# Optimization experiments

Measured on AMD Instinct MI355X. Metric: run time of the kernel, lower is better.

Reference implementation:

```python
import jax, jax.numpy as jnp
import numpy as np

BETA = 0.25  # commitment loss weight


def setup_inputs() -> dict:
    key = jax.random.key(0)
    ks = jax.random.split(key, 6)
    B, H, W, C = 16, 64, 64, 128
    x = jax.random.normal(ks[0], (B, H, W, C), dtype=jnp.float32)
    # dictionaries: sizes 2^6 .. 2^9 (from num_embeddings=[64,512]),
    # keras RandomUniform default init in (-0.05, 0.05)
    dicts = {}
    for i, n_emb in enumerate([64, 128, 256, 512]):
        dicts[f"dict{i}"] = jax.random.uniform(
            ks[i + 1], (C, n_emb), dtype=jnp.float32, minval=-0.05, maxval=0.05)
    vq_alpha = jnp.asarray(1.0, dtype=jnp.float32)
    vq_gamma = jnp.full((4,), 0.25, dtype=jnp.float32)  # 1/num_dictionaries
    return {"x": x, **dicts, "vq_alpha": vq_alpha, "vq_gamma": vq_gamma}


def _vq_pass(flat, D):
    # flat: [N, C], D: [C, K]. Squared-euclidean distances then argmin.
    dist = (jnp.sum(flat * flat, axis=1, keepdims=True)
            + jnp.sum(D * D, axis=0)[None, :]
            - 2.0 * (flat @ D))  # [N, K]
    idx = jnp.argmin(dist, axis=1)  # [N]
    # one_hot @ D.T  ==  gather rows of D.T
    return jnp.take(D.T, idx, axis=0)  # [N, C]


def reference(x, dict0, dict1, dict2, dict3, vq_alpha, vq_gamma):
    dicts = [dict0, dict1, dict2, dict3]
    C = x.shape[-1]
    flat = x.reshape(-1, C)  # [N, C]
    weighted_q = jnp.zeros_like(x)
    dictionary_loss = jnp.asarray(0.0, x.dtype)
    commitment_loss = jnp.asarray(0.0, x.dtype)
    for i, D in enumerate(dicts):
        q = (vq_alpha * _vq_pass(flat, D)).reshape(x.shape)
        weighted_q = weighted_q + vq_gamma[i] * q
        dictionary_loss += vq_gamma[i] * jnp.mean(
            jnp.square(jax.lax.stop_gradient(x) - q))
        commitment_loss += vq_gamma[i] * jnp.mean(
            jnp.square(x - jax.lax.stop_gradient(q)))
    loss = dictionary_loss + BETA * commitment_loss
    # straight-through estimator
    out = x + jax.lax.stop_gradient(weighted_q - x)
    return out, loss
```

## Files before the change

### kernel.cpp

```cpp
#include <hip/hip_runtime.h>

#define CDIM 128
#define NC   8388608

typedef __attribute__((ext_vector_type(8)))  short bf8v;
typedef __attribute__((ext_vector_type(16))) float f32x16;


__device__ __forceinline__ void bsplit(float v, short& h, short& lo) {
  unsigned u = __float_as_uint(v);
  unsigned hb = (u + 0x7fffu + ((u >> 16) & 1u)) >> 16;
  float hf = __uint_as_float(hb << 16);
  float lf = v - hf;
  unsigned u2 = __float_as_uint(lf);
  unsigned lb = (u2 + 0x7fffu + ((u2 >> 16) & 1u)) >> 16;
  h = (short)hb; lo = (short)lb;
}

__global__ void vq_prep(const float* __restrict__ D0, const float* __restrict__ D1,
                        const float* __restrict__ D2, const float* __restrict__ D3,
                        float* __restrict__ nrm, float* __restrict__ DT,
                        bf8v* __restrict__ Bph, bf8v* __restrict__ Bpl) {
  const int b = blockIdx.x;
  if (b < 60) {
    int g = b * 256 + threadIdx.x;
    int T = g >> 9, c = (g >> 6) & 7, l = g & 63;
    int col = T * 32 + (l & 31);
    int k0 = c * 16 + (l >> 5) * 8;
    const float* D; int K, cb;
    if (col < 64)       { D = D0; K = 64;  cb = col; }
    else if (col < 192) { D = D1; K = 128; cb = col - 64; }
    else if (col < 448) { D = D2; K = 256; cb = col - 192; }
    else                { D = D3; K = 512; cb = col - 448; }
    short h0,h1,h2,h3,h4,h5,h6,h7, q0,q1,q2,q3,q4,q5,q6,q7;
    bsplit(D[(k0+0)*K + cb], h0, q0);
    bsplit(D[(k0+1)*K + cb], h1, q1);
    bsplit(D[(k0+2)*K + cb], h2, q2);
    bsplit(D[(k0+3)*K + cb], h3, q3);
    bsplit(D[(k0+4)*K + cb], h4, q4);
    bsplit(D[(k0+5)*K + cb], h5, q5);
    bsplit(D[(k0+6)*K + cb], h6, q6);
    bsplit(D[(k0+7)*K + cb], h7, q7);
    Bph[g] = (bf8v){h0,h1,h2,h3,h4,h5,h6,h7};
    Bpl[g] = (bf8v){q0,q1,q2,q3,q4,q5,q6,q7};
  } else {
    int g = (b - 60) * 256 + threadIdx.x;
    if (g >= 960) return;
    const float* D; int K, k; float* T;
    if (g < 64)       { D = D0; K = 64;  k = g;       T = DT; }
    else if (g < 192) { D = D1; K = 128; k = g - 64;  T = DT + 8192; }
    else if (g < 448) { D = D2; K = 256; k = g - 192; T = DT + 24576; }
    else              { D = D3; K = 512; k = g - 448; T = DT + 57344; }
    float s = 0.f;
    for (int c = 0; c < 128; ++c) { float v = D[c*K+k]; s = fmaf(v,v,s); T[k*128+c] = v; }
    nrm[g] = s;
  }
}

#define MK8(U0, U1, HD, LD) { \
  short h0,h1,h2,h3,h4,h5,h6,h7, q0,q1,q2,q3,q4,q5,q6,q7; \
  bsplit(U0.x,h0,q0); bsplit(U0.y,h1,q1); bsplit(U0.z,h2,q2); bsplit(U0.w,h3,q3); \
  bsplit(U1.x,h4,q4); bsplit(U1.y,h5,q5); bsplit(U1.z,h6,q6); bsplit(U1.w,h7,q7); \
  HD = (bf8v){h0,h1,h2,h3,h4,h5,h6,h7}; \
  LD = (bf8v){q0,q1,q2,q3,q4,q5,q6,q7}; }

#define MFMA32(AC, AF, BF) AC = __builtin_amdgcn_mfma_f32_32x32x16_bf16((AF), (BF), (AC), 0, 0, 0)

#define PF_T(TT) { \
  const bf8v* __restrict__ gh = Bph + (TT) * 512; \
  const bf8v* __restrict__ gl = Bpl + (TT) * 512; \
  pf0 = gh[t]; pf1 = gh[256 + t]; pf2 = gl[t]; pf3 = gl[256 + t]; }

#define STORE_T(BF) { \
  BL[BF][t] = pf0; BL[BF][256 + t] = pf1; BL[BF][512 + t] = pf2; BL[BF][768 + t] = pf3; }

#define COMPUTE_T(T, BF) { \
  f32x16 ae = zero16, ao = zero16; \
  _Pragma("unroll") \
  for (int cp = 0; cp < 4; ++cp) { \
    const int ce = 2*cp, co = 2*cp+1; \
    bf8v bhe = BL[BF][ce*64 + l]; bf8v bho = BL[BF][co*64 + l]; \
    bf8v ble = BL[BF][512 + ce*64 + l]; bf8v blo = BL[BF][512 + co*64 + l]; \
    MFMA32(ae, Ah[ce], bhe); MFMA32(ao, Ah[co], bho); \
    MFMA32(ae, Al[ce], bhe); MFMA32(ao, Al[co], bho); \
    MFMA32(ae, Ah[ce], ble); MFMA32(ao, Ah[co], blo); \
  } \
  f32x16 sv = ae + ao; \
  const float nv = nrm_g[(T)*32 + (l & 31)]; \
  const int colT = (T)*32 + (l & 31); \
  _Pragma("unroll") \
  for (int r = 0; r < 16; ++r) { \
    float c0 = fmaf(-2.f, sv[r], nv); \
    if (c0 < bc[r]) { bc[r] = c0; bk[r] = colT; } } }

#define ROUND_T(T) { \
  if ((T) < 29) { \
    STORE_T(((T) + 1) & 1); \
    const int TN = ((T) + 2 <= 29) ? (T) + 2 : 29; \
    PF_T(TN); \
  } \
  COMPUTE_T(T, (T) & 1) \
  __syncthreads(); }

#define FLUSHG(DICTID, BASE, GAM) { \
  _Pragma("unroll") \
  for (int r = 0; r < 16; ++r) { \
    float b0 = bc[r]; int K0 = bk[r]; \
    _Pragma("unroll") \
    for (int m = 1; m <= 16; m <<= 1) { \
      float pb = __shfl_xor(b0, m); int pk = __shfl_xor(K0, m); \
      if (pb < b0 || (pb == b0 && pk < K0)) { b0 = pb; K0 = pk; } } \
    if ((l & 31) == 0) { \
      const int ro = (r & 3) + 8 * (r >> 2) + 4 * hl; \
      keys[((rowbase + ro) << 2) | (DICTID)] = K0 - (BASE); \
      const float nst = nrm_g[K0]; \
       \
      lossacc = fmaf((GAM) * a, fmaf(am1, nst, b0), lossacc); } \
    bc[r] = 1e30f; bk[r] = 0; } }

__global__ __launch_bounds__(256, 2) void vq_mfma(
    const float* __restrict__ x,
    const bf8v* __restrict__ Bph, const bf8v* __restrict__ Bpl,
    const float* __restrict__ nrm_g,
    const float* __restrict__ alpha_p, const float* __restrict__ gamma_p,
    int* __restrict__ keys, float* __restrict__ partials)
{
  __shared__ bf8v  BL[2][1024];
  __shared__ float lossW[4];

  const int t = threadIdx.x;
  const int w = t >> 6, l = t & 63;
  const int hl = l >> 5;
  const int rowbase = blockIdx.x * 128 + w * 32;

  const float a   = alpha_p[0];
  const float am1 = a - 1.f;
  const float g0 = gamma_p[0], g1 = gamma_p[1], g2 = gamma_p[2], g3 = gamma_p[3];
  const float gsum = g0 + g1 + g2 + g3;

  bf8v Ah[8], Al[8];
  float xsqh = 0.f;
  {
    const float* __restrict__ xr = x + (size_t)(rowbase + (l & 31)) * CDIM + hl * 8;
    #pragma unroll
    for (int c = 0; c < 8; ++c) {
      float4 u0 = *(const float4*)(xr + c * 16);
      float4 u1 = *(const float4*)(xr + c * 16 + 4);
      xsqh = fmaf(u0.x,u0.x, xsqh); xsqh = fmaf(u0.y,u0.y, xsqh);
      xsqh = fmaf(u0.z,u0.z, xsqh); xsqh = fmaf(u0.w,u0.w, xsqh);
      xsqh = fmaf(u1.x,u1.x, xsqh); xsqh = fmaf(u1.y,u1.y, xsqh);
      xsqh = fmaf(u1.z,u1.z, xsqh); xsqh = fmaf(u1.w,u1.w, xsqh);
      MK8(u0, u1, Ah[c], Al[c])
    }
  }
  float xs_ = xsqh;
  #pragma unroll
  for (int m = 1; m <= 32; m <<= 1) xs_ += __shfl_xor(xs_, m);

  f32x16 zero16;
  #pragma unroll
  for (int i = 0; i < 16; ++i) zero16[i] = 0.f;

  float bc[16]; int bk[16];
  #pragma unroll
  for (int r = 0; r < 16; ++r) { bc[r] = 1e30f; bk[r] = 0; }
  float lossacc = 0.f;

  bf8v pf0, pf1, pf2, pf3;
  PF_T(0)
  STORE_T(0)
  PF_T(1)
  __syncthreads();

  ROUND_T(0) ROUND_T(1)
  FLUSHG(0, 0, g0)
  for (int T = 2; T < 6; ++T) ROUND_T(T)
  FLUSHG(1, 64, g1)
  for (int T = 6; T < 14; ++T) ROUND_T(T)
  FLUSHG(2, 192, g2)
  for (int T = 14; T < 30; ++T) ROUND_T(T)
  FLUSHG(3, 448, g3)

  {
    float wl = lossacc + __shfl_xor(lossacc, 32);
    if (l == 0) lossW[w] = fmaf(gsum, xs_, wl);
  }
  __syncthreads();
  if (t == 0) partials[blockIdx.x] = lossW[0] + lossW[1] + lossW[2] + lossW[3];
}

__global__ __launch_bounds__(256, 8) void vq_merge(
    const float* __restrict__ DT, const int* __restrict__ keys,
    const float* __restrict__ alpha_p, const float* __restrict__ gamma_p,
    float* __restrict__ out)
{
  __shared__ int kk[32][4];
  const int t = threadIdx.x;
  const int row0 = blockIdx.x * 32;
  if (t < 128) kk[t >> 2][t & 3] = keys[((row0 + (t >> 2)) << 2) | (t & 3)];
  __syncthreads();
  const float a = alpha_p[0];
  const float g0 = gamma_p[0], g1 = gamma_p[1], g2 = gamma_p[2], g3 = gamma_p[3];
  #pragma unroll
  for (int j = 0; j < 4; ++j) {
    const int f = j * 256 + t;
    const int r = f >> 5, c4 = (f & 31) * 4;
    const size_t off = (size_t)(row0 + r) * CDIM + c4;
    const float4 d0 = *(const float4*)(DT +         kk[r][0] * 128 + c4);
    const float4 d1 = *(const float4*)(DT +  8192 + kk[r][1] * 128 + c4);
    const float4 d2 = *(const float4*)(DT + 24576 + kk[r][2] * 128 + c4);
    const float4 d3 = *(const float4*)(DT + 57344 + kk[r][3] * 128 + c4);
    float4 o;
    o.x = a * (g0*d0.x + g1*d1.x + g2*d2.x + g3*d3.x);
    o.y = a * (g0*d0.y + g1*d1.y + g2*d2.y + g3*d3.y);
    o.z = a * (g0*d0.z + g1*d1.z + g2*d2.z + g3*d3.z);
    o.w = a * (g0*d0.w + g1*d1.w + g2*d2.w + g3*d3.w);
    *(float4*)(out + off) = o;
  }
}

__global__ void vq_loss(const float* __restrict__ partials, float* __restrict__ lossp) {
  __shared__ float wr[4];
  const int t = threadIdx.x;
  float v = partials[t] + partials[t + 256];
  #pragma unroll
  for (int off = 32; off > 0; off >>= 1) v += __shfl_down(v, off);
  if ((t & 63) == 0) wr[t >> 6] = v;
  __syncthreads();
  if (t == 0) lossp[0] = (wr[0] + wr[1] + wr[2] + wr[3]) * (1.25f / 8388608.f);
}

extern "C" void kernel_launch(void* const* d_in, const int* in_sizes, int n_in,
                              void* d_out, int out_size, void* d_ws, size_t ws_size,
                              hipStream_t stream) {
  const float* x  = (const float*)d_in[0];
  const float* D0 = (const float*)d_in[1];
  const float* D1 = (const float*)d_in[2];
  const float* D2 = (const float*)d_in[3];
  const float* D3 = (const float*)d_in[4];
  const float* alpha = (const float*)d_in[5];
  const float* gamma = (const float*)d_in[6];
  float* out = (float*)d_out;

  float* ws  = (float*)d_ws;
  float* nrm = ws;
  float* DT  = ws + 1024;
  bf8v*  Bph = (bf8v*)(ws + 123904);
  bf8v*  Bpl = (bf8v*)(ws + 185344);
  int*  keys = (int*)(ws + 246784);
  float* partials = ws + 508928;

  vq_prep<<<64, 256, 0, stream>>>(D0, D1, D2, D3, nrm, DT, Bph, Bpl);
  vq_mfma<<<512, 256, 0, stream>>>(x, Bph, Bpl, nrm, alpha, gamma, keys, partials);
  vq_merge<<<2048, 256, 0, stream>>>(DT, keys, alpha, gamma, out);
  vq_loss<<<1, 256, 0, stream>>>(partials, out + NC);
}
```

Before: 99.56 us.

## Split channel reduction across wave pairs and halve rows per block

Each block now covers 64 rows instead of 128. The two waves assigned to the same 32-row tile each multiply half of the channel chunks and exchange partial accumulators through a new LDS buffer. The kh==0 wave then does the argmin scan and flush. This halves the per-wave A-fragment registers, raises launch bounds to 3 waves per SIMD and doubles the grid to 1024 blocks, aiming for better occupancy and latency hiding. In exchange, every codebook tile is staged into LDS twice as often in total, there is an extra LDS round-trip per tile, and half the waves sit idle during the comparison phase. The loss reduction is widened to sum 1024 partials.

```diff
diff --git a/kernel.cpp b/kernel.cpp
--- a/kernel.cpp
+++ b/kernel.cpp
@@ -74,33 +74,40 @@
 #define STORE_T(BF) { \
   BL[BF][t] = pf0; BL[BF][256 + t] = pf1; BL[BF][512 + t] = pf2; BL[BF][768 + t] = pf3; }
 
-#define COMPUTE_T(T, BF) { \
-  f32x16 ae = zero16, ao = zero16; \
+#define COMPUTE_H(T, BF) { \
+  f32x16 acc = zero16; \
   _Pragma("unroll") \
   for (int cp = 0; cp < 4; ++cp) { \
-    const int ce = 2*cp, co = 2*cp+1; \
-    bf8v bhe = BL[BF][ce*64 + l]; bf8v bho = BL[BF][co*64 + l]; \
-    bf8v ble = BL[BF][512 + ce*64 + l]; bf8v blo = BL[BF][512 + co*64 + l]; \
-    MFMA32(ae, Ah[ce], bhe); MFMA32(ao, Ah[co], bho); \
-    MFMA32(ae, Al[ce], bhe); MFMA32(ao, Al[co], bho); \
-    MFMA32(ae, Ah[ce], ble); MFMA32(ao, Ah[co], blo); \
+    const int cc = 2 * cp + kh; \
+    bf8v bh = BL[BF][cc * 64 + l]; \
+    bf8v bq = BL[BF][512 + cc * 64 + l]; \
+    MFMA32(acc, Ah[cp], bh); \
+    MFMA32(acc, Al[cp], bh); \
+    MFMA32(acc, Ah[cp], bq); \
   } \
-  f32x16 sv = ae + ao; \
-  const float nv = nrm_g[(T)*32 + (l & 31)]; \
-  const int colT = (T)*32 + (l & 31); \
+  if (kh == 1) { \
+    _Pragma("unroll") \
+    for (int i = 0; i < 16; ++i) XCf[(T) & 1][rt][i][l] = acc[i]; \
+  } else { aeK = acc; } }
+
+#define CRIT_T(T) { \
+  const float nv = nrm_g[(T) * 32 + (l & 31)]; \
+  const int colT = (T) * 32 + (l & 31); \
   _Pragma("unroll") \
   for (int r = 0; r < 16; ++r) { \
-    float c0 = fmaf(-2.f, sv[r], nv); \
+    float sv = aeK[r] + XCf[(T) & 1][rt][r][l]; \
+    float c0 = fmaf(-2.f, sv, nv); \
     if (c0 < bc[r]) { bc[r] = c0; bk[r] = colT; } } }
 
-#define ROUND_T(T) { \
+#define RND_K(T) { \
   if ((T) < 29) { \
     STORE_T(((T) + 1) & 1); \
     const int TN = ((T) + 2 <= 29) ? (T) + 2 : 29; \
     PF_T(TN); \
   } \
-  COMPUTE_T(T, (T) & 1) \
-  __syncthreads(); }
+  COMPUTE_H(T, (T) & 1) \
+  __syncthreads(); \
+  if (kh == 0) { CRIT_T(T) } }
 
 #define FLUSHG(DICTID, BASE, GAM) { \
   _Pragma("unroll") \
@@ -114,11 +121,10 @@
       const int ro = (r & 3) + 8 * (r >> 2) + 4 * hl; \
       keys[((rowbase + ro) << 2) | (DICTID)] = K0 - (BASE); \
       const float nst = nrm_g[K0]; \
-       \
       lossacc = fmaf((GAM) * a, fmaf(am1, nst, b0), lossacc); } \
     bc[r] = 1e30f; bk[r] = 0; } }
 
-__global__ __launch_bounds__(256, 2) void vq_mfma(
+__global__ __launch_bounds__(256, 3) void vq_mfma(
     const float* __restrict__ x,
     const bf8v* __restrict__ Bph, const bf8v* __restrict__ Bpl,
     const float* __restrict__ nrm_g,
@@ -126,31 +132,35 @@
     int* __restrict__ keys, float* __restrict__ partials)
 {
   __shared__ bf8v  BL[2][1024];
+  __shared__ float XCf[2][2][16][64];
   __shared__ float lossW[4];
 
   const int t = threadIdx.x;
   const int w = t >> 6, l = t & 63;
   const int hl = l >> 5;
-  const int rowbase = blockIdx.x * 128 + w * 32;
+  const int rt = w & 1;
+  const int kh = w >> 1;
+  const int rowbase = blockIdx.x * 64 + rt * 32;
 
   const float a   = alpha_p[0];
   const float am1 = a - 1.f;
   const float g0 = gamma_p[0], g1 = gamma_p[1], g2 = gamma_p[2], g3 = gamma_p[3];
   const float gsum = g0 + g1 + g2 + g3;
 
-  bf8v Ah[8], Al[8];
+  bf8v Ah[4], Al[4];
   float xsqh = 0.f;
   {
     const float* __restrict__ xr = x + (size_t)(rowbase + (l & 31)) * CDIM + hl * 8;
     #pragma unroll
-    for (int c = 0; c < 8; ++c) {
-      float4 u0 = *(const float4*)(xr + c * 16);
-      float4 u1 = *(const float4*)(xr + c * 16 + 4);
+    for (int cp = 0; cp < 4; ++cp) {
+      const int cc = 2 * cp + kh;
+      float4 u0 = *(const float4*)(xr + cc * 16);
+      float4 u1 = *(const float4*)(xr + cc * 16 + 4);
       xsqh = fmaf(u0.x,u0.x, xsqh); xsqh = fmaf(u0.y,u0.y, xsqh);
       xsqh = fmaf(u0.z,u0.z, xsqh); xsqh = fmaf(u0.w,u0.w, xsqh);
       xsqh = fmaf(u1.x,u1.x, xsqh); xsqh = fmaf(u1.y,u1.y, xsqh);
       xsqh = fmaf(u1.z,u1.z, xsqh); xsqh = fmaf(u1.w,u1.w, xsqh);
-      MK8(u0, u1, Ah[c], Al[c])
+      MK8(u0, u1, Ah[cp], Al[cp])
     }
   }
   float xs_ = xsqh;
@@ -160,6 +170,7 @@
   f32x16 zero16;
   #pragma unroll
   for (int i = 0; i < 16; ++i) zero16[i] = 0.f;
+  f32x16 aeK = zero16;
 
   float bc[16]; int bk[16];
   #pragma unroll
@@ -172,14 +183,18 @@
   PF_T(1)
   __syncthreads();
 
-  ROUND_T(0) ROUND_T(1)
-  FLUSHG(0, 0, g0)
-  for (int T = 2; T < 6; ++T) ROUND_T(T)
-  FLUSHG(1, 64, g1)
-  for (int T = 6; T < 14; ++T) ROUND_T(T)
-  FLUSHG(2, 192, g2)
-  for (int T = 14; T < 30; ++T) ROUND_T(T)
-  FLUSHG(3, 448, g3)
+  RND_K(0) RND_K(1)
+  if (kh == 0) { FLUSHG(0, 0, g0) }
+  RND_K(2) RND_K(3) RND_K(4) RND_K(5)
+  if (kh == 0) { FLUSHG(1, 64, g1) }
+  RND_K(6) RND_K(7) RND_K(8) RND_K(9)
+  RND_K(10) RND_K(11) RND_K(12) RND_K(13)
+  if (kh == 0) { FLUSHG(2, 192, g2) }
+  RND_K(14) RND_K(15) RND_K(16) RND_K(17)
+  RND_K(18) RND_K(19) RND_K(20) RND_K(21)
+  RND_K(22) RND_K(23) RND_K(24) RND_K(25)
+  RND_K(26) RND_K(27) RND_K(28) RND_K(29)
+  if (kh == 0) { FLUSHG(3, 448, g3) }
 
   {
     float wl = lossacc + __shfl_xor(lossacc, 32);
@@ -222,7 +237,7 @@
 __global__ void vq_loss(const float* __restrict__ partials, float* __restrict__ lossp) {
   __shared__ float wr[4];
   const int t = threadIdx.x;
-  float v = partials[t] + partials[t + 256];
+  float v = partials[t] + partials[t + 256] + partials[t + 512] + partials[t + 768];
   #pragma unroll
   for (int off = 32; off > 0; off >>= 1) v += __shfl_down(v, off);
   if ((t & 63) == 0) wr[t >> 6] = v;
@@ -251,7 +266,7 @@
   float* partials = ws + 508928;
 
   vq_prep<<<64, 256, 0, stream>>>(D0, D1, D2, D3, nrm, DT, Bph, Bpl);
-  vq_mfma<<<512, 256, 0, stream>>>(x, Bph, Bpl, nrm, alpha, gamma, keys, partials);
+  vq_mfma<<<1024, 256, 0, stream>>>(x, Bph, Bpl, nrm, alpha, gamma, keys, partials);
   vq_merge<<<2048, 256, 0, stream>>>(DT, keys, alpha, gamma, out);
   vq_loss<<<1, 256, 0, stream>>>(partials, out + NC);
 }
```

New measurement: 194.4 us. 1.95x slower.
